# Kernel optimization log

Hardware: AMD Instinct MI355X
Metric: run time of the kernel (lower is better)

## Reference

```python
import jax, jax.numpy as jnp
import numpy as np

NUM_HEADS = 16
EMBED_DIM = 1024
HEAD_SIZE = EMBED_DIM // NUM_HEADS


def setup_inputs() -> dict:
    key = jax.random.key(0)
    ks = jax.random.split(key, 9)
    B, S, D = 4, 2048, EMBED_DIM
    scale = 1.0 / np.sqrt(D)
    x = jax.random.normal(ks[0], (B, S, D), dtype=jnp.float32)
    Wq = jax.random.normal(ks[1], (D, D), dtype=jnp.float32) * scale
    bq = jnp.zeros((D,), dtype=jnp.float32)
    Wk = jax.random.normal(ks[2], (D, D), dtype=jnp.float32) * scale
    bk = jnp.zeros((D,), dtype=jnp.float32)
    Wv = jax.random.normal(ks[3], (D, D), dtype=jnp.float32) * scale
    bv = jnp.zeros((D,), dtype=jnp.float32)
    Wo = jax.random.normal(ks[4], (D, D), dtype=jnp.float32) * scale
    bo = jnp.zeros((D,), dtype=jnp.float32)
    return {"x": x, "Wq": Wq, "bq": bq, "Wk": Wk, "bk": bk,
            "Wv": Wv, "bv": bv, "Wo": Wo, "bo": bo}


def reference(x, Wq, bq, Wk, bk, Wv, bv, Wo, bo):
    B, S, D = x.shape
    H, Hd = NUM_HEADS, HEAD_SIZE

    def split_heads(t):  # [B,S,D] -> [B,H,S,Hd]
        return t.reshape(B, S, H, Hd).transpose(0, 2, 1, 3)

    q = split_heads(x @ Wq + bq)
    k = split_heads(x @ Wk + bk)
    v = split_heads(x @ Wv + bv)

    scores = jnp.einsum("bhqd,bhkd->bhqk", q, k) / np.sqrt(Hd)
    probs = jax.nn.softmax(scores, axis=-1)  # dropout rate=0 -> identity
    ctx = jnp.einsum("bhqk,bhkd->bhqd", probs, v)
    ctx = ctx.transpose(0, 2, 1, 3).reshape(B, S, D)
    return ctx @ Wo + bo
```

## Files before the change

### kernel.cpp

```cpp
#include <hip/hip_runtime.h>
#include <cstdint>


typedef unsigned short ushort_t;
typedef __attribute__((ext_vector_type(8))) short short8;
typedef __attribute__((ext_vector_type(4))) float f32x4;

constexpr int Bn = 4, Sn = 2048, Dn = 1024, Hn = 16;
constexpr int Mn = Bn * Sn;
constexpr float QSCALE = 0.125f * 1.44269504088896340736f;

__device__ __forceinline__ ushort_t f2b(float f) {
    union { float f; unsigned u; } v; v.f = f;
    unsigned u = v.u;
    return (ushort_t)((u + 0x7fffu + ((u >> 16) & 1u)) >> 16);
}

__device__ __forceinline__ unsigned cvt_pk_bf16(float lo, float hi) {
    unsigned r;
    asm("v_cvt_pk_bf16_f32 %0, %1, %2" : "=v"(r) : "v"(lo), "v"(hi));
    return r;
}

__device__ __forceinline__ float exp2_hw(float x) {
    float y;
    asm("v_exp_f32 %0, %1" : "=v"(y) : "v"(x));
    return y;
}

__device__ __forceinline__ void gl_lds16(const void* g, void* l) {
    __builtin_amdgcn_global_load_lds(
        (const __attribute__((address_space(1))) unsigned int*)g,
        (__attribute__((address_space(3))) unsigned int*)l, 16, 0, 0);
}

__global__ void cast_f32_bf16(const float* __restrict__ in, ushort_t* __restrict__ out, int n4) {
    int i = blockIdx.x * blockDim.x + threadIdx.x;
    if (i < n4) {
        float4 f = ((const float4*)in)[i];
        ushort4 o;
        o.x = f2b(f.x); o.y = f2b(f.y); o.z = f2b(f.z); o.w = f2b(f.w);
        ((ushort4*)out)[i] = o;
    }
}

__global__ void transpose_cast_w(const float* __restrict__ W, ushort_t* __restrict__ Wt, int dim) {
    __shared__ float tile[32][33];
    int bx = blockIdx.x * 32;
    int by = blockIdx.y * 32;
    int tx = threadIdx.x, ty = threadIdx.y;
    for (int i = 0; i < 32; i += 8)
        tile[ty + i][tx] = W[(size_t)(by + ty + i) * dim + bx + tx];
    __syncthreads();
    for (int i = 0; i < 32; i += 8)
        Wt[(size_t)(bx + ty + i) * dim + by + tx] = f2b(tile[tx][ty + i]);
}

__global__ void transpose_v(const ushort_t* __restrict__ V, ushort_t* __restrict__ Vt) {
    __shared__ ushort_t tile[64][72];
    int s0 = blockIdx.x * 64;
    int bh = blockIdx.y;
    int b = bh >> 4, h = bh & 15;
    int t = threadIdx.x;
    for (int j = 0; j < 16; ++j) {
        int idx = t + j * 256;
        int r = idx >> 6, c = idx & 63;
        tile[r][c] = V[(size_t)(b * Sn + s0 + r) * Dn + h * 64 + c];
    }
    __syncthreads();
    for (int j = 0; j < 16; ++j) {
        int idx = t + j * 256;
        int d = idx >> 6, c = idx & 63;
        Vt[(size_t)(bh * 64 + d) * Sn + s0 + c] = tile[c][d];
    }
}

template <int OUTF32, int QKVSEL>
__global__ __launch_bounds__(256) void gemm_bt(
    const ushort_t* __restrict__ A, const ushort_t* __restrict__ Bt,
    const float* __restrict__ b0, const float* __restrict__ b1, const float* __restrict__ b2,
    void* __restrict__ Cv, int Mq, int Nq, int Kq, float osc0, int nbx) {
    alignas(16) __shared__ ushort_t Al[128 * 64];
    alignas(16) __shared__ ushort_t Bl[128 * 64];
    const int tid = threadIdx.x;
    const int l = tid & 63, wid = tid >> 6;
    const int lo = l & 15, g = l >> 4;
    const int wm = wid >> 1, wn = wid & 1;
    const int per_xcd = (int)gridDim.x >> 3;
    const int virt = ((int)blockIdx.x & 7) * per_xcd + ((int)blockIdx.x >> 3);
    const int m0 = (virt / nbx) * 128, n0g = (virt % nbx) * 128;
    int sel = QKVSEL ? (n0g >> 10) : 0;
    const float* bias = QKVSEL ? (sel == 0 ? b0 : (sel == 1 ? b1 : b2)) : b0;
    float oscale = (QKVSEL && sel != 0) ? 1.0f : osc0;
    const int n0 = QKVSEL ? (n0g & 1023) : n0g;

    const int rr = l >> 3, cc = l & 7;

    f32x4 acc[4][4];
    for (int a = 0; a < 4; ++a)
        for (int b = 0; b < 4; ++b) acc[a][b] = f32x4{0.f, 0.f, 0.f, 0.f};

    for (int kt = 0; kt < Kq; kt += 64) {
        __syncthreads();
#pragma unroll
        for (int i = 0; i < 4; ++i) {
            int row = wid * 32 + i * 8 + rr;
            gl_lds16(&A[(size_t)(m0 + row) * Kq + kt + cc * 8], &Al[(wid * 32 + i * 8) * 64]);
            gl_lds16(&Bt[(size_t)(n0g + row) * Kq + kt + cc * 8], &Bl[(wid * 32 + i * 8) * 64]);
        }
        __syncthreads();
#pragma unroll
        for (int ks = 0; ks < 2; ++ks) {
            short8 af[4], bf[4];
#pragma unroll
            for (int mi = 0; mi < 4; ++mi)
                af[mi] = *(const short8*)&Al[(wm * 64 + mi * 16 + lo) * 64 + ks * 32 + g * 8];
#pragma unroll
            for (int ni = 0; ni < 4; ++ni)
                bf[ni] = *(const short8*)&Bl[(wn * 64 + ni * 16 + lo) * 64 + ks * 32 + g * 8];
            __builtin_amdgcn_s_setprio(1);
#pragma unroll
            for (int mi = 0; mi < 4; ++mi)
#pragma unroll
                for (int ni = 0; ni < 4; ++ni)
                    acc[mi][ni] = __builtin_amdgcn_mfma_f32_16x16x32_bf16(af[mi], bf[ni], acc[mi][ni], 0, 0, 0);
            __builtin_amdgcn_s_setprio(0);
        }
    }
    for (int mi = 0; mi < 4; ++mi) {
        int row = m0 + wm * 64 + mi * 16 + g * 4;
        for (int ni = 0; ni < 4; ++ni) {
            int col = n0 + wn * 64 + ni * 16 + lo;
            float bcol = bias ? bias[col] : 0.f;
            for (int i = 0; i < 4; ++i) {
                float v = (acc[mi][ni][i] + bcol) * oscale;
                if (OUTF32)
                    ((float*)Cv)[(size_t)(row + i) * Nq + col] = v;
                else
                    ((ushort_t*)Cv)[(size_t)sel * Mn * Dn + (size_t)(row + i) * Nq + col] = f2b(v);
            }
        }
    }
}

__global__ __launch_bounds__(512, 4) void attn_kernel(
    const ushort_t* __restrict__ Qg, const ushort_t* __restrict__ Kg,
    const ushort_t* __restrict__ Vtg, ushort_t* __restrict__ Ctx) {
    alignas(16) __shared__ ushort_t Kl[2][64 * 64];
    alignas(16) __shared__ ushort_t Vl[2][64 * 64];
    alignas(16) __shared__ ushort_t Pl[8][32 * 64];
    const int tid = threadIdx.x;
    const int l = tid & 63, wid = tid >> 6;
    const int lo = l & 15, g = l >> 4;
    const int virt = (blockIdx.x & 7) * 64 + (blockIdx.x >> 3);
    const int bh = virt >> 3, qc = virt & 7;
    const int b = bh >> 4, h = bh & 15;
    const int q0 = qc * 256 + wid * 32;
    constexpr int NT = Sn / 64;

    short8 qf[2][2];
#pragma unroll
    for (int qi = 0; qi < 2; ++qi) {
        size_t qrow = (size_t)(b * Sn + q0 + qi * 16 + lo);
#pragma unroll
        for (int ks = 0; ks < 2; ++ks)
            qf[qi][ks] = *(const short8*)&Qg[qrow * Dn + h * 64 + ks * 32 + g * 8];
    }

    const int rr = l >> 3, cc = l & 7;
    const int swc = ((cc ^ rr) << 4);
    const char* gK = (const char*)(Kg + (size_t)(b * Sn) * Dn + h * 64);
    const char* gV = (const char*)(Vtg + (size_t)(bh * 64) * Sn);

    float ls[2] = {0.f, 0.f};
    f32x4 ctx[2][4];
#pragma unroll
    for (int qi = 0; qi < 2; ++qi)
#pragma unroll
        for (int ni = 0; ni < 4; ++ni) ctx[qi][ni] = f32x4{0.f, 0.f, 0.f, 0.f};

    char* Pw = (char*)Pl[wid];

#define STAGE_KV(T, BUF)                                                                 \
    {                                                                                    \
        int row = wid * 8 + rr;                                                          \
        gl_lds16(gK + ((size_t)((T)*64 + row) * Dn) * 2 + swc,                           \
                 &Kl[BUF][(wid * 8) * 64]);                                              \
        gl_lds16(gV + ((size_t)row * Sn + (size_t)(T)*64) * 2 + swc,                     \
                 &Vl[BUF][(wid * 8) * 64]);                                              \
    }

    STAGE_KV(0, 0);

    for (int t = 0; t < NT; ++t) {
        const char* Kb = (const char*)Kl[t & 1];
        const char* Vb = (const char*)Vl[t & 1];
        asm volatile("s_waitcnt vmcnt(0)" ::: "memory");
        __builtin_amdgcn_s_barrier();
        __builtin_amdgcn_sched_barrier(0);
        if (t + 1 < NT) STAGE_KV(t + 1, (t + 1) & 1);

        f32x4 sa[2][4];
#pragma unroll
        for (int qi = 0; qi < 2; ++qi)
#pragma unroll
            for (int ni = 0; ni < 4; ++ni) sa[qi][ni] = f32x4{0.f, 0.f, 0.f, 0.f};
#pragma unroll
        for (int ks = 0; ks < 2; ++ks) {
            short8 kf[4];
#pragma unroll
            for (int ni = 0; ni < 4; ++ni) {
                int row = ni * 16 + lo;
                kf[ni] = *(const short8*)(Kb + ((row * 128 + ks * 64 + g * 16) ^ ((lo & 7) << 4)));
            }
            __builtin_amdgcn_s_setprio(1);
#pragma unroll
            for (int qi = 0; qi < 2; ++qi)
#pragma unroll
                for (int ni = 0; ni < 4; ++ni)
                    sa[qi][ni] = __builtin_amdgcn_mfma_f32_16x16x32_bf16(kf[ni], qf[qi][ks], sa[qi][ni], 0, 0, 0);
            __builtin_amdgcn_s_setprio(0);
        }

#pragma unroll
        for (int qi = 0; qi < 2; ++qi) {
            float rs = 0.f;
#pragma unroll
            for (int ni = 0; ni < 4; ++ni)
#pragma unroll
                for (int i = 0; i < 4; ++i) {
                    sa[qi][ni][i] = exp2_hw(sa[qi][ni][i]);
                    rs += sa[qi][ni][i];
                }
            rs += __shfl_xor(rs, 16);
            rs += __shfl_xor(rs, 32);
            ls[qi] += rs;
#pragma unroll
            for (int ni = 0; ni < 4; ++ni) {
                uint2 w;
                w.x = cvt_pk_bf16(sa[qi][ni][0], sa[qi][ni][1]);
                w.y = cvt_pk_bf16(sa[qi][ni][2], sa[qi][ni][3]);
                unsigned byte = (unsigned)(((qi * 16 + lo) * 128 + (ni * 16 + g * 4) * 2) ^ ((lo & 7) << 4));
                *(uint2*)(Pw + byte) = w;
            }
        }
        asm volatile("s_waitcnt lgkmcnt(0)" ::: "memory");
        __builtin_amdgcn_sched_barrier(0);

#pragma unroll
        for (int ks = 0; ks < 2; ++ks) {
            short8 vf[4];
#pragma unroll
            for (int ni = 0; ni < 4; ++ni) {
                int row = ni * 16 + lo;
                vf[ni] = *(const short8*)(Vb + ((row * 128 + ks * 64 + g * 16) ^ ((lo & 7) << 4)));
            }
            short8 pa[2];
#pragma unroll
            for (int qi = 0; qi < 2; ++qi)
                pa[qi] = *(const short8*)(Pw + (((qi * 16 + lo) * 128 + ks * 64 + g * 16) ^ ((lo & 7) << 4)));
            __builtin_amdgcn_s_setprio(1);
#pragma unroll
            for (int qi = 0; qi < 2; ++qi)
#pragma unroll
                for (int ni = 0; ni < 4; ++ni)
                    ctx[qi][ni] = __builtin_amdgcn_mfma_f32_16x16x32_bf16(pa[qi], vf[ni], ctx[qi][ni], 0, 0, 0);
            __builtin_amdgcn_s_setprio(0);
        }
    }
#undef STAGE_KV

#pragma unroll
    for (int qi = 0; qi < 2; ++qi) {
        float linv = 1.0f / ls[qi];
#pragma unroll
        for (int i = 0; i < 4; ++i) {
            float lrow = __shfl(linv, g * 4 + i);
            int prow = qi * 16 + g * 4 + i;
#pragma unroll
            for (int ni = 0; ni < 4; ++ni) {
                unsigned byte = (unsigned)((prow * 128 + (ni * 16 + lo) * 2) ^ ((prow & 7) << 4));
                *(ushort_t*)(Pw + byte) = f2b(ctx[qi][ni][i] * lrow);
            }
        }
    }
    asm volatile("s_waitcnt lgkmcnt(0)" ::: "memory");
    __builtin_amdgcn_sched_barrier(0);
#pragma unroll
    for (int j = 0; j < 4; ++j) {
        int row = j * 8 + rr;
        uint4 w = *(const uint4*)(Pw + ((row * 128 + cc * 16) ^ ((row & 7) << 4)));
        *(uint4*)&Ctx[(size_t)(b * Sn + q0 + row) * Dn + h * 64 + cc * 8] = w;
    }
}

extern "C" void kernel_launch(void* const* d_in, const int* in_sizes, int n_in,
                              void* d_out, int out_size, void* d_ws, size_t ws_size,
                              hipStream_t stream) {
    const float* x  = (const float*)d_in[0];
    const float* Wq = (const float*)d_in[1];
    const float* bq = (const float*)d_in[2];
    const float* Wk = (const float*)d_in[3];
    const float* bk = (const float*)d_in[4];
    const float* Wv = (const float*)d_in[5];
    const float* bv = (const float*)d_in[6];
    const float* Wo = (const float*)d_in[7];
    const float* bo = (const float*)d_in[8];

    ushort_t* ws = (ushort_t*)d_ws;
    const size_t MD = (size_t)Mn * Dn;
    const size_t DD = (size_t)Dn * Dn;
    ushort_t* xb  = ws;
    ushort_t* wqt = xb + MD;
    ushort_t* wkt = wqt + DD;
    ushort_t* wvt = wkt + DD;
    ushort_t* wot = wvt + DD;
    ushort_t* qb  = wot + DD;
    ushort_t* kb  = qb + MD;
    ushort_t* vb  = kb + MD;
    ushort_t* vt  = vb + MD;
    ushort_t* cx  = vt + MD;

    int n4 = (int)(MD / 4);
    cast_f32_bf16<<<(n4 + 255) / 256, 256, 0, stream>>>(x, xb, n4);
    dim3 tg(Dn / 32, Dn / 32), tb(32, 8);
    transpose_cast_w<<<tg, tb, 0, stream>>>(Wq, wqt, Dn);
    transpose_cast_w<<<tg, tb, 0, stream>>>(Wk, wkt, Dn);
    transpose_cast_w<<<tg, tb, 0, stream>>>(Wv, wvt, Dn);
    transpose_cast_w<<<tg, tb, 0, stream>>>(Wo, wot, Dn);
    gemm_bt<0, 1><<<dim3(1536), 256, 0, stream>>>(
        xb, wqt, bq, bk, bv, qb, Mn, Dn, Dn, QSCALE, 24);
    transpose_v<<<dim3(Sn / 64, Bn * Hn), 256, 0, stream>>>(vb, vt);
    attn_kernel<<<dim3(512), 512, 0, stream>>>(qb, kb, vt, cx);
    gemm_bt<1, 0><<<dim3(512), 256, 0, stream>>>(
        cx, wot, bo, nullptr, nullptr, (float*)d_out, Mn, Dn, Dn, 1.0f, 8);
}
```

Before: 227.6 us.

## Batch weight transposes into one launch and defer softmax row-sum reductions

The four weight transpose-cast launches are merged into a single launch that uses blockIdx.z to pick the matrix, which removes three kernel launch overheads. In the attention loop, V fragments for both k-steps are loaded before the exp step so the LDS reads overlap with the softmax work. The per-tile cross-lane shuffle reduction of row sums is moved out of the loop and done once at the end, with four independent partial accumulators. The cost is more live registers for vf and pa, which could lower occupancy.

```diff
diff --git a/kernel.cpp b/kernel.cpp
--- a/kernel.cpp
+++ b/kernel.cpp
@@ -44,8 +44,15 @@
     }
 }
 
-__global__ void transpose_cast_w(const float* __restrict__ W, ushort_t* __restrict__ Wt, int dim) {
+__global__ void transpose_cast_w4(
+    const float* __restrict__ W0, const float* __restrict__ W1,
+    const float* __restrict__ W2, const float* __restrict__ W3,
+    ushort_t* __restrict__ T0, ushort_t* __restrict__ T1,
+    ushort_t* __restrict__ T2, ushort_t* __restrict__ T3, int dim) {
     __shared__ float tile[32][33];
+    int z = blockIdx.z;
+    const float* W = z == 0 ? W0 : (z == 1 ? W1 : (z == 2 ? W2 : W3));
+    ushort_t* Wt = z == 0 ? T0 : (z == 1 ? T1 : (z == 2 ? T2 : T3));
     int bx = blockIdx.x * 32;
     int by = blockIdx.y * 32;
     int tx = threadIdx.x, ty = threadIdx.y;
@@ -222,19 +229,26 @@
             __builtin_amdgcn_s_setprio(0);
         }
 
+        short8 vf[2][4];
+#pragma unroll
+        for (int ks = 0; ks < 2; ++ks)
+#pragma unroll
+            for (int ni = 0; ni < 4; ++ni) {
+                int row = ni * 16 + lo;
+                vf[ks][ni] = *(const short8*)(Vb + ((row * 128 + ks * 64 + g * 16) ^ ((lo & 7) << 4)));
+            }
+
 #pragma unroll
         for (int qi = 0; qi < 2; ++qi) {
-            float rs = 0.f;
-#pragma unroll
-            for (int ni = 0; ni < 4; ++ni)
-#pragma unroll
-                for (int i = 0; i < 4; ++i) {
-                    sa[qi][ni][i] = exp2_hw(sa[qi][ni][i]);
-                    rs += sa[qi][ni][i];
-                }
-            rs += __shfl_xor(rs, 16);
-            rs += __shfl_xor(rs, 32);
-            ls[qi] += rs;
+            float r0 = 0.f, r1 = 0.f, r2 = 0.f, r3 = 0.f;
+#pragma unroll
+            for (int i = 0; i < 4; ++i) {
+                sa[qi][0][i] = exp2_hw(sa[qi][0][i]); r0 += sa[qi][0][i];
+                sa[qi][1][i] = exp2_hw(sa[qi][1][i]); r1 += sa[qi][1][i];
+                sa[qi][2][i] = exp2_hw(sa[qi][2][i]); r2 += sa[qi][2][i];
+                sa[qi][3][i] = exp2_hw(sa[qi][3][i]); r3 += sa[qi][3][i];
+            }
+            ls[qi] += (r0 + r1) + (r2 + r3);
 #pragma unroll
             for (int ni = 0; ni < 4; ++ni) {
                 uint2 w;
@@ -247,32 +261,30 @@
         asm volatile("s_waitcnt lgkmcnt(0)" ::: "memory");
         __builtin_amdgcn_sched_barrier(0);
 
-#pragma unroll
-        for (int ks = 0; ks < 2; ++ks) {
-            short8 vf[4];
-#pragma unroll
-            for (int ni = 0; ni < 4; ++ni) {
-                int row = ni * 16 + lo;
-                vf[ni] = *(const short8*)(Vb + ((row * 128 + ks * 64 + g * 16) ^ ((lo & 7) << 4)));
-            }
-            short8 pa[2];
+        short8 pa[2][2];
+#pragma unroll
+        for (int qi = 0; qi < 2; ++qi)
+#pragma unroll
+            for (int ks = 0; ks < 2; ++ks)
+                pa[qi][ks] = *(const short8*)(Pw + (((qi * 16 + lo) * 128 + ks * 64 + g * 16) ^ ((lo & 7) << 4)));
+        __builtin_amdgcn_s_setprio(1);
+#pragma unroll
+        for (int ks = 0; ks < 2; ++ks)
 #pragma unroll
             for (int qi = 0; qi < 2; ++qi)
-                pa[qi] = *(const short8*)(Pw + (((qi * 16 + lo) * 128 + ks * 64 + g * 16) ^ ((lo & 7) << 4)));
-            __builtin_amdgcn_s_setprio(1);
-#pragma unroll
-            for (int qi = 0; qi < 2; ++qi)
 #pragma unroll
                 for (int ni = 0; ni < 4; ++ni)
-                    ctx[qi][ni] = __builtin_amdgcn_mfma_f32_16x16x32_bf16(pa[qi], vf[ni], ctx[qi][ni], 0, 0, 0);
-            __builtin_amdgcn_s_setprio(0);
-        }
+                    ctx[qi][ni] = __builtin_amdgcn_mfma_f32_16x16x32_bf16(pa[qi][ks], vf[ks][ni], ctx[qi][ni], 0, 0, 0);
+        __builtin_amdgcn_s_setprio(0);
     }
 #undef STAGE_KV
 
 #pragma unroll
     for (int qi = 0; qi < 2; ++qi) {
-        float linv = 1.0f / ls[qi];
+        float lsum = ls[qi];
+        lsum += __shfl_xor(lsum, 16);
+        lsum += __shfl_xor(lsum, 32);
+        float linv = 1.0f / lsum;
 #pragma unroll
         for (int i = 0; i < 4; ++i) {
             float lrow = __shfl(linv, g * 4 + i);
@@ -323,11 +335,8 @@
 
     int n4 = (int)(MD / 4);
     cast_f32_bf16<<<(n4 + 255) / 256, 256, 0, stream>>>(x, xb, n4);
-    dim3 tg(Dn / 32, Dn / 32), tb(32, 8);
-    transpose_cast_w<<<tg, tb, 0, stream>>>(Wq, wqt, Dn);
-    transpose_cast_w<<<tg, tb, 0, stream>>>(Wk, wkt, Dn);
-    transpose_cast_w<<<tg, tb, 0, stream>>>(Wv, wvt, Dn);
-    transpose_cast_w<<<tg, tb, 0, stream>>>(Wo, wot, Dn);
+    transpose_cast_w4<<<dim3(Dn / 32, Dn / 32, 4), dim3(32, 8), 0, stream>>>(
+        Wq, Wk, Wv, Wo, wqt, wkt, wvt, wot, Dn);
     gemm_bt<0, 1><<<dim3(1536), 256, 0, stream>>>(
         xb, wqt, bq, bk, bv, qb, Mn, Dn, Dn, QSCALE, 24);
     transpose_v<<<dim3(Sn / 64, Bn * Hn), 256, 0, stream>>>(vb, vt);
```

Result: slower. 373.2 us (+64.0%).
